# Kernel optimization log

Measured on AMD Instinct MI355X. Metric: run time of the kernel, lower is better.

## Reference

```python
import jax, jax.numpy as jnp
import numpy as np

V = 50000      # tokenizer vocab size
E = 128        # embedding_dim
H = 160        # encoder_hidden_dim (bidirectional -> 2H)
D = 196        # decoder_hidden_dim
A = 224        # attention_dim
BN = 56        # bottle_neck_dim
PAD, START, END, UNK = 0, 1, 2, 3
COV_FACTOR = 0.75


def _lstm_step(x, h, c, Wi, Wh, bi, bh):
    # torch gate order: i, f, g, o
    g = x @ Wi.T + h @ Wh.T + bi + bh
    i, f, gg, o = jnp.split(g, 4, axis=-1)
    c = jax.nn.sigmoid(f) * c + jax.nn.sigmoid(i) * jnp.tanh(gg)
    h = jax.nn.sigmoid(o) * jnp.tanh(c)
    return h, c


def _run_lstm(x_tbe, Wi, Wh, bi, bh):
    B = x_tbe.shape[1]
    Hh = Wh.shape[1]
    def step(carry, xt):
        h, c = carry
        h, c = _lstm_step(xt, h, c, Wi, Wh, bi, bh)
        return (h, c), h
    init = (jnp.zeros((B, Hh), x_tbe.dtype), jnp.zeros((B, Hh), x_tbe.dtype))
    (hT, cT), hs = jax.lax.scan(step, init, x_tbe)
    return hs, hT, cT


def setup_inputs() -> dict:
    key = jax.random.key(0)
    ks = iter(jax.random.split(key, 48))
    def rn(shape, s=0.05):
        return jax.random.normal(next(ks), shape, jnp.float32) * s
    B, Tin, Ttgt = 32, 256, 100
    inp = {
        'batch_input_ids': jax.random.randint(next(ks), (B, Tin), 0, V + 50, dtype=jnp.int32),
        'batch_target_ids': jax.random.randint(next(ks), (B, Ttgt), 0, V + 50, dtype=jnp.int32),
        'max_num_oovs': 50,
        'emb': rn((V, E), 0.1),
        # bidirectional encoder LSTM
        'Wi_f': rn((4 * H, E)), 'Wh_f': rn((4 * H, H)),
        'bi_f': jnp.zeros(4 * H), 'bh_f': jnp.zeros(4 * H),
        'Wi_b': rn((4 * H, E)), 'Wh_b': rn((4 * H, H)),
        'bi_b': jnp.zeros(4 * H), 'bh_b': jnp.zeros(4 * H),
        # enc->dec bridges
        'Weh': rn((D, 2 * H)), 'beh': jnp.zeros(D),
        'Wec': rn((D, 2 * H)), 'bec': jnp.zeros(D),
        # decoder LSTMCell
        'Wi_d': rn((4 * D, E)), 'Wh_d': rn((4 * D, D)),
        'bi_d': jnp.zeros(4 * D), 'bh_d': jnp.zeros(4 * D),
        # attention
        'Wea': rn((A, 2 * H)), 'bea': jnp.zeros(A),
        'Wda': rn((A, D)),
        'Wca': rn((A, 1)),
        'v_attn': rn((1, A)),
        # vocab projection (bottleneck)
        'W1': rn((BN, D + 2 * H)), 'b1': jnp.zeros(BN),
        'W2': rn((V - END, BN)), 'b2': jnp.zeros(V - END),
        # p_gen switch
        'Wcs': rn((1, 2 * H)), 'bcs': jnp.zeros(1),
        'Wds': rn((1, D)),
        'Wes': rn((1, E)),
    }
    return inp


def reference(batch_input_ids, batch_target_ids, max_num_oovs, emb,
              Wi_f, Wh_f, bi_f, bh_f, Wi_b, Wh_b, bi_b, bh_b,
              Weh, beh, Wec, bec, Wi_d, Wh_d, bi_d, bh_d,
              Wea, bea, Wda, Wca, v_attn, W1, b1, W2, b2,
              Wcs, bcs, Wds, Wes):
    B, Tin = batch_input_ids.shape
    # map OOV input ids to <unk> for embedding lookup
    in_mapped = jnp.where(batch_input_ids >= V, UNK, batch_input_ids)
    x_tbe = emb[in_mapped].transpose(1, 0, 2)          # [Tin,B,E]
    hs_f, hTf, cTf = _run_lstm(x_tbe, Wi_f, Wh_f, bi_f, bh_f)
    hs_b, hTb, cTb = _run_lstm(x_tbe[::-1], Wi_b, Wh_b, bi_b, bh_b)
    enc = jnp.concatenate([hs_f, hs_b[::-1]], -1).transpose(1, 0, 2)  # [B,Tin,2H]
    h = jnp.concatenate([hTf, hTb], -1) @ Weh.T + beh   # [B,D]
    c = jnp.concatenate([cTf, cTb], -1) @ Wec.T + bec   # [B,D]
    enc_attn = enc @ Wea.T + bea                        # [B,Tin,A] (loop-invariant)
    pad_mask = batch_input_ids == PAD
    wca = Wca[:, 0]                                     # [A]
    cov0 = jnp.zeros((B, Tin))
    cur0 = jnp.full((B,), START, jnp.int32)

    def step(carry, nt):
        h, c, cov, cur, nll, cl = carry
        e = emb[cur]                                     # [B,E]
        h, c = _lstm_step(e, h, c, Wi_d, Wh_d, bi_d, bh_d)
        s = jnp.tanh(enc_attn + (h @ Wda.T)[:, None, :] + cov[:, :, None] * wca)
        s = s @ v_attn[0]                                # [B,Tin]
        s = jnp.where(pad_mask, -jnp.inf, s)
        attn = jax.nn.softmax(s, axis=1)                 # [B,Tin]
        ctx = jnp.einsum('bt,bth->bh', attn, enc)        # [B,2H]
        hc = jnp.concatenate([h, ctx], -1)
        vocab = jax.nn.softmax(jnp.tanh(hc @ W1.T + b1) @ W2.T + b2, axis=1)  # [B,V-END]
        p_gen = jax.nn.sigmoid(ctx @ Wcs[0] + bcs[0] + h @ Wds[0] + e @ Wes[0])  # [B]
        # F.pad(vocab, (END, max_num_oovs)).gather(1, nt): left-pad END zeros,
        # right-pad OOV zeros -> gen prob is vocab[nt-END] if END<=nt<V else 0
        idx = jnp.clip(nt - END, 0, vocab.shape[1] - 1)
        gen_p = jnp.take_along_axis(vocab, idx[:, None], axis=1)[:, 0]
        gen_p = jnp.where((nt >= END) & (nt < V), gen_p, 0.0)
        copy_p = jnp.sum(attn * (batch_input_ids == nt[:, None]), axis=1)
        p = p_gen * gen_p + (1.0 - p_gen) * copy_p
        nll = nll - jnp.log(p + 1e-9)
        cl = cl + jnp.minimum(attn, cov).sum(axis=1)
        cov = cov + attn
        cur = jnp.where(nt >= V, UNK, nt)
        return (h, c, cov, cur, nll, cl), None

    (h, c, cov, cur, nll, cl), _ = jax.lax.scan(
        step, (h, c, cov0, cur0, jnp.zeros(B), jnp.zeros(B)), batch_target_ids.T)
    nll_loss = nll.sum()
    cov_loss = cl.sum()
    return nll_loss, cov_loss, nll_loss + COV_FACTOR * cov_loss
```

## Files before the change

kernel.cpp:

```cpp
#include <hip/hip_runtime.h>

#define MSCOPE __HIP_MEMORY_SCOPE_AGENT


constexpr size_t oXf   = 0;
constexpr size_t oXb   = oXf   + (size_t)8192*640;
constexpr size_t oXd   = oXb   + (size_t)8192*640;
constexpr size_t oHencB= oXd   + (size_t)3200*784;
constexpr size_t oEncA = oHencB+ (size_t)64*256*160;
constexpr size_t oEs   = oEncA + (size_t)8192*224;
constexpr size_t oCT   = oEs   + 3200;
constexpr size_t oH0   = oCT   + 10240;
constexpr size_t oC0   = oH0   + 6272;
constexpr size_t oHWdsAll = oC0 + 6272;
constexpr size_t oCtxWAll = oHWdsAll + 3200;
constexpr size_t oCopyAll = oCtxWAll + 3200;
constexpr size_t oZidxAll = oCopyAll + 3200;
constexpr size_t oClAll   = oZidxAll + 3200;
constexpr size_t oNllWg   = oClAll + 32;
constexpr size_t oW1cT    = oNllWg + 224;
constexpr size_t oFEnd    = oW1cT + 17920;
constexpr size_t oHdAll   = 0;
constexpr size_t oUAll    = oHdAll + (size_t)100*6272;
constexpr size_t oUPreAll = oUAll  + (size_t)100*1792;
constexpr size_t oHwdaAll = oUPreAll + (size_t)100*1792;
constexpr size_t oPartAll = oHwdaAll + (size_t)100*7168;
#define ENCW(d,t)  (((d)*256 + (t))*16)
#define FLSTM(s)   (8192 + (s)*16)
#define FAUX(s)    (9792 + (s)*16)
#define FP2W(s,m)  (11392 + (s)*64 + (m)*16)
#define CP3        17792
#define CFIN       17793
constexpr int fEnd = 17800;
constexpr unsigned ENC_FULL  = 0xFFFFFu;
constexpr unsigned LSTM_FULL = 0x1FFFFFFu;
constexpr unsigned AUX_FULL  = 0xFFu;
constexpr unsigned P2_FULL   = 0xFFFFFFFFu;

__device__ __forceinline__ float fast_tanh(float x){
  float e = __expf(-2.f*fabsf(x));
  float r = (1.f - e) * __builtin_amdgcn_rcpf(1.f + e);
  return copysignf(r, x);
}
__device__ __forceinline__ float sigm(float x){
  return __builtin_amdgcn_rcpf(1.f + __expf(-x));
}
__device__ __forceinline__ float aload(const float* p){
  return __hip_atomic_load(const_cast<float*>(p), __ATOMIC_RELAXED, MSCOPE);
}
__device__ __forceinline__ float2 aload2(const float* p){
  unsigned long long u = __hip_atomic_load(
      reinterpret_cast<unsigned long long*>(const_cast<float*>(p)),
      __ATOMIC_RELAXED, MSCOPE);
  float2 r; __builtin_memcpy(&r, &u, 8); return r;
}
__device__ __forceinline__ void astore(float* p, float v){
  __hip_atomic_store(p, v, __ATOMIC_RELAXED, MSCOPE);
}
template<int SLP>
__device__ __forceinline__ void wait_mask(unsigned* word, unsigned target, int tid){
  if (tid == 0){
    while (__hip_atomic_load(word, __ATOMIC_RELAXED, MSCOPE) != target)
      __builtin_amdgcn_s_sleep(SLP);
  }
  __syncthreads();
}
__device__ __forceinline__ void or_bit(unsigned* word, unsigned bit){
  (void)__hip_atomic_fetch_or(word, bit, __ATOMIC_RELAXED, MSCOPE);
}
__device__ __forceinline__ void add1(unsigned* word){
  (void)__hip_atomic_fetch_add(word, 1u, __ATOMIC_RELAXED, MSCOPE);
}
__device__ __forceinline__ float block_sum(float v, float* red){
  #pragma unroll
  for (int o=32;o;o>>=1) v += __shfl_down(v,o);
  if ((threadIdx.x&63)==0) red[threadIdx.x>>6] = v;
  __syncthreads();
  v = red[0]+red[1]+red[2]+red[3];
  __syncthreads();
  return v;
}

__global__ void prep_kernel(const int* __restrict__ in_ids, const int* __restrict__ tgt,
                            int* __restrict__ in_mapped, int* __restrict__ cur_ids,
                            unsigned* __restrict__ flags){
  int i = blockIdx.x*256 + threadIdx.x;
  if (i < 8192){
    int t = i >> 5, b = i & 31;
    int id = in_ids[b*256 + t];
    in_mapped[i] = (id >= 50000) ? 3 : id;
  }
  if (i < 3200){
    int k = i >> 5, b = i & 31;
    int id = (k == 0) ? 1 : tgt[b*100 + (k-1)];
    cur_ids[i] = (id >= 50000) ? 3 : id;
  }
  if (i < fEnd) flags[i] = 0u;
}

__global__ void w1c_transpose(const float* __restrict__ W1, float* __restrict__ W1cT){
  int i = blockIdx.x*256 + threadIdx.x;
  if (i < 17920){ int q = i / 56, g = i - q*56; W1cT[q*56+g] = W1[(size_t)g*516 + 196 + q]; }
}

struct RGArgs{ const int* gid; const float* emb; const float* W;
               const float* bias1; const float* bias2; float* out; int N; };
__global__ void __launch_bounds__(256) rowgemm(RGArgs a){
  __shared__ float rl[8*128];
  const int tid = threadIdx.x;
  const int N = a.N;
  const size_t r0 = (size_t)blockIdx.x*8;
  const size_t t = r0 >> 5; const int b0 = (int)(r0 & 31);
  for (int i = tid; i < 8*128; i += 256){
    int r = i >> 7, k = i & 127;
    rl[i] = a.emb[(size_t)a.gid[r0+r]*128 + k];
  }
  __syncthreads();
  for (int g = tid; g < N; g += 256){
    const float* wr = a.W + (size_t)g*128;
    float acc[8];
    #pragma unroll
    for (int r=0;r<8;r++) acc[r]=0.f;
    for (int k=0;k<128;k+=4){
      float4 wv = *(const float4*)(wr+k);
      #pragma unroll
      for (int r=0;r<8;r++){
        float4 xv = *(const float4*)(rl + r*128 + k);
        acc[r] += wv.x*xv.x + wv.y*xv.y + wv.z*xv.z + wv.w*xv.w;
      }
    }
    float bias = a.bias1[g] + a.bias2[g];
    float* op = a.out + ((size_t)t*N + g)*32 + b0;
    *(float4*)(op)   = make_float4(acc[0]+bias,acc[1]+bias,acc[2]+bias,acc[3]+bias);
    *(float4*)(op+4) = make_float4(acc[4]+bias,acc[5]+bias,acc[6]+bias,acc[7]+bias);
  }
}

__global__ void es_kernel(const int* __restrict__ gid, const float* __restrict__ emb,
                          const float* __restrict__ Wes, float* __restrict__ es){
  int r = blockIdx.x, l = threadIdx.x;
  const float* e = emb + (size_t)gid[r]*128;
  float acc = e[l]*Wes[l] + e[l+64]*Wes[l+64];
  #pragma unroll
  for (int o=32;o;o>>=1) acc += __shfl_down(acc,o);
  if (l==0) es[r] = acc;
}

struct EncArgs{ const float* Xf; const float* Xb; const float* Whf; const float* Whb;
                float* hencB; float* cT; unsigned* flg; };
__global__ void __launch_bounds__(256) enc_scan(EncArgs a){
  extern __shared__ float sm[];
  float* Wl = sm;
  float* hl = sm + 5120;
  const int wg = blockIdx.x;
  const int dir = wg/20, jwg = wg%20;
  const int tid = threadIdx.x;
  const int b = tid & 31, jl = tid >> 5;
  const int j = jwg*8 + jl;
  const float* Wh = dir ? a.Whb : a.Whf;
  const float* X  = dir ? a.Xb  : a.Xf;
  float* HB = a.hencB + (size_t)dir*32*256*160;
  unsigned* flg = a.flg;
  for (int i = tid; i < 32*160; i += 256){
    int row = i/160, k = i - row*160;
    int gate = row >> 3, jj = row & 7;
    Wl[i] = Wh[((size_t)(gate*160 + jwg*8 + jj))*160 + k];
  }
  for (int i = tid; i < 32*164; i += 256) hl[i] = 0.f;
  float c = 0.f;
  const float4* w0 = (const float4*)(Wl + (0*8+jl)*160);
  const float4* w1 = (const float4*)(Wl + (1*8+jl)*160);
  const float4* w2 = (const float4*)(Wl + (2*8+jl)*160);
  const float4* w3 = (const float4*)(Wl + (3*8+jl)*160);
  __syncthreads();
  for (int t = 0; t < 256; ++t){
    const int trow = dir ? 255 - t : t;
    const float* xr = X + ((size_t)trow*640 + j)*32 + b;
    float g0 = xr[0], g1 = xr[5120], g2 = xr[10240], g3 = xr[15360];
    if (t > 0){
      wait_mask<2>(flg + ENCW(dir, t-1), ENC_FULL, tid);
      const int tprev = dir ? (256 - t) : (t-1);
      for (int i2 = tid; i2 < 2560; i2 += 256){
        int bb = i2/80, kk = (i2 - bb*80)*2;
        float2 v = aload2(HB + ((size_t)bb*256 + tprev)*160 + kk);
        *(float2*)(hl + bb*164 + kk) = v;
      }
    }
    __syncthreads();
    const float4* hr = (const float4*)(hl + b*164);
    #pragma unroll 4
    for (int q = 0; q < 40; ++q){
      float4 hv = hr[q];
      float4 a0 = w0[q], a1 = w1[q], a2 = w2[q], a3 = w3[q];
      g0 += hv.x*a0.x + hv.y*a0.y + hv.z*a0.z + hv.w*a0.w;
      g1 += hv.x*a1.x + hv.y*a1.y + hv.z*a1.z + hv.w*a1.w;
      g2 += hv.x*a2.x + hv.y*a2.y + hv.z*a2.z + hv.w*a2.w;
      g3 += hv.x*a3.x + hv.y*a3.y + hv.z*a3.z + hv.w*a3.w;
    }
    float ig = sigm(g0), fg = sigm(g1), gc = fast_tanh(g2), og = sigm(g3);
    c = fg*c + ig*gc;
    float h = og * fast_tanh(c);
    astore(&HB[((size_t)b*256 + trow)*160 + j], h);
    __syncthreads();
    if (tid == 0) or_bit(flg + ENCW(dir, t), 1u << jwg);
  }
  a.cT[dir*5120 + b*160 + j] = c;
}

__global__ void mid_kernel(const float* __restrict__ hencB, const float* __restrict__ cT,
                           const float* __restrict__ Weh, const float* __restrict__ beh,
                           const float* __restrict__ Wec, const float* __restrict__ bec,
                           float* __restrict__ h0, float* __restrict__ c0){
  __shared__ float hc[320], cc[320];
  int b = blockIdx.x, tid = threadIdx.x;
  if (tid < 160){
    hc[tid]     = hencB[((size_t)b*256 + 255)*160 + tid];
    hc[160+tid] = hencB[((size_t)(32+b)*256 + 0)*160 + tid];
    cc[tid]     = cT[b*160 + tid];
    cc[160+tid] = cT[5120 + b*160 + tid];
  }
  __syncthreads();
  for (int g = tid; g < 196; g += 256){
    const float* w1 = Weh + (size_t)g*320;
    const float* w2 = Wec + (size_t)g*320;
    float a1 = beh[g], a2 = bec[g];
    for (int k = 0; k < 320; ++k){ a1 += hc[k]*w1[k]; a2 += cc[k]*w2[k]; }
    h0[b*196 + g] = a1;
    c0[b*196 + g] = a2;
  }
}

__global__ void __launch_bounds__(256) encA_gemm(const float* __restrict__ hencB,
                 const float* __restrict__ Wea, const float* __restrict__ bea,
                 float* __restrict__ encA){
  __shared__ float rl[8*320];
  const int tid = threadIdx.x;
  const size_t r0 = (size_t)blockIdx.x*8;
  for (int i = tid; i < 8*320; i += 256){
    int r = i/320, k = i - r*320;
    size_t row = r0 + r; int b = (int)(row >> 8), t = (int)(row & 255);
    rl[i] = (k < 160) ? hencB[((size_t)b*256 + t)*160 + k]
                      : hencB[((size_t)(32+b)*256 + t)*160 + (k-160)];
  }
  __syncthreads();
  for (int g = tid; g < 224; g += 256){
    const float* wr = Wea + (size_t)g*320;
    float acc[8];
    #pragma unroll
    for (int r=0;r<8;r++) acc[r]=0.f;
    for (int k=0;k<320;k+=4){
      float4 wv = *(const float4*)(wr+k);
      #pragma unroll
      for (int r=0;r<8;r++){
        float4 xv = *(const float4*)(rl + r*320 + k);
        acc[r] += wv.x*xv.x + wv.y*xv.y + wv.z*xv.z + wv.w*xv.w;
      }
    }
    float bias = bea[g];
    #pragma unroll
    for (int r=0;r<8;r++) encA[(r0+r)*224 + g] = acc[r] + bias;
  }
}

struct DecArgs{
  const float* Xd; const float* hencB; const float* encA;
  const float* h0; const float* c0;
  const float* Whd; const float* Wda; const float* Wca; const float* vat;
  const float* W1; const float* b1; const float* W1cT; const float* W2; const float* b2;
  const float* Wcs; const float* bcs; const float* Wds; const float* es;
  const int* in_ids; const int* tgt;
  float* hdAll; float* uAll; float* uPreAll; float* hwdaAll;
  float* hWdsAll; float* ctxWAll; float* copyAll;
  float* zidxAll; float* partAll; float* clAll; float* nllWg; float* out;
  unsigned* flg;
};

__device__ __forceinline__ void load_scr(const float* hp, float* scr, int tid){
  for (int i2 = tid; i2 < 3136; i2 += 256){
    float2 hv = aload2(hp + i2*2);
    int e = i2*2; int b2 = e & 31; int j2 = e >> 5;
    scr[b2*204 + j2]     = hv.x;
    scr[(b2+1)*204 + j2] = hv.y;
  }
}

__global__ void __launch_bounds__(256) dec_scan(DecArgs A){
  extern __shared__ float sm[];
  const int wg = blockIdx.x, tid = threadIdx.x;
  const int bp = tid & 31, jl = tid >> 5;
  unsigned* flg = A.flg;

  if (wg < 25){
    const int wl = wg;
    const int j = wl*8 + jl;
    float* Wl  = sm;
    float* scr = sm + 6272;
    for (int i = tid; i < 32*196; i += 256){
      int row = i/196, k = i - row*196;
      int gate = row >> 3, jj = row & 7;
      int jg = wl*8 + jj;
      Wl[i] = (jg < 196) ? A.Whd[((size_t)(gate*196 + jg))*196 + k] : 0.f;
    }
    float c = (j < 196) ? A.c0[bp*196 + j] : 0.f;
    for (int i = tid; i < 6272; i += 256){
      int bb = i/196, k = i - bb*196;
      scr[bb*204 + k] = A.h0[i];
    }
    const float4* w0 = (const float4*)(Wl + (0*8+jl)*196);
    const float4* w1 = (const float4*)(Wl + (1*8+jl)*196);
    const float4* w2 = (const float4*)(Wl + (2*8+jl)*196);
    const float4* w3 = (const float4*)(Wl + (3*8+jl)*196);
    __syncthreads();
    for (int s = 0; s < 100; ++s){
      float x0=0.f,x1=0.f,x2=0.f,x3=0.f;
      if (j < 196){
        const float* xr = A.Xd + ((size_t)s*784 + j)*32 + bp;
        x0 = xr[0]; x1 = xr[6272]; x2 = xr[12544]; x3 = xr[18816];
      }
      if (s > 0){
        wait_mask<2>(flg + FLSTM(s-1), LSTM_FULL, tid);
        load_scr(A.hdAll + (size_t)(s-1)*6272, scr, tid);
      }
      __syncthreads();
      if (j < 196){
        float g0=x0,g1=x1,g2=x2,g3=x3;
        const float4* hr = (const float4*)(scr + bp*204);
        #pragma unroll 7
        for (int q = 0; q < 49; ++q){
          float4 hv = hr[q];
          float4 a0 = w0[q], a1 = w1[q], a2 = w2[q], a3 = w3[q];
          g0 += hv.x*a0.x + hv.y*a0.y + hv.z*a0.z + hv.w*a0.w;
          g1 += hv.x*a1.x + hv.y*a1.y + hv.z*a1.z + hv.w*a1.w;
          g2 += hv.x*a2.x + hv.y*a2.y + hv.z*a2.z + hv.w*a2.w;
          g3 += hv.x*a3.x + hv.y*a3.y + hv.z*a3.z + hv.w*a3.w;
        }
        float ig = sigm(g0), fg = sigm(g1), gc = fast_tanh(g2), og = sigm(g3);
        c = fg*c + ig*gc;
        float h = og * fast_tanh(c);
        astore(&A.hdAll[(size_t)s*6272 + j*32 + bp], h);
      }
      __syncthreads();
      if (tid == 0) or_bit(flg + FLSTM(s), 1u << wl);
    }
    return;
  }

  if (wg < 33){
    const int a_ = wg - 25;
    float* wdaL = sm;
    float* w1hL = sm + 5488;
    float* WdsL = sm + 6860;
    float* scr  = sm + 7056;
    for (int i = tid; i < 28*196; i += 256){
      int al = i/196, k = i - al*196;
      wdaL[i] = A.Wda[(size_t)(a_*28 + al)*196 + k];
    }
    for (int i = tid; i < 7*196; i += 256){
      int gl = i/196, k = i - gl*196;
      w1hL[i] = A.W1[(size_t)(a_*7 + gl)*516 + k];
    }
    if (a_ == 7) for (int i = tid; i < 196; i += 256) WdsL[i] = A.Wds[i];
    __syncthreads();
    for (int s = 0; s < 100; ++s){
      wait_mask<2>(flg + FLSTM(s), LSTM_FULL, tid);
      load_scr(A.hdAll + (size_t)s*6272, scr, tid);
      __syncthreads();
      for (int i = tid; i < 896; i += 256){
        int b2 = i & 31, al = i >> 5;
        const float4* h4 = (const float4*)(scr + b2*204);
        const float4* w4 = (const float4*)(wdaL + al*196);
        float acc = 0.f;
        #pragma unroll 7
        for (int q = 0; q < 49; ++q){
          float4 a4 = h4[q], b4 = w4[q];
          acc += a4.x*b4.x + a4.y*b4.y + a4.z*b4.z + a4.w*b4.w;
        }
        astore(&A.hwdaAll[(size_t)s*7168 + b2*224 + a_*28 + al], acc);
      }
      if (tid < 224){
        int b2 = tid & 31, gl = tid >> 5;
        int g = a_*7 + gl;
        const float4* h4 = (const float4*)(scr + b2*204);
        const float4* w4 = (const float4*)(w1hL + gl*196);
        float acc = A.b1[g];
        #pragma unroll 7
        for (int q = 0; q < 49; ++q){
          float4 a4 = h4[q], b4 = w4[q];
          acc += a4.x*b4.x + a4.y*b4.y + a4.z*b4.z + a4.w*b4.w;
        }
        astore(&A.uPreAll[(size_t)s*1792 + b2*56 + g], acc);
      }
      if (a_ == 7 && tid < 32){
        const float* hb = scr + tid*204;
        float acc = 0.f;
        #pragma unroll 4
        for (int q = 0; q < 196; ++q) acc += hb[q]*WdsL[q];
        astore(&A.hWdsAll[s*32 + tid], acc);
      }
      __syncthreads();
      if (tid == 0) or_bit(flg + FAUX(s), 1u << a_);
    }
    return;
  }

  if (wg < 65){
    const int b = wg - 33;
    float* hwdaL = sm;
    float* attnL = sm + 224;
    float* pctx  = sm + 480;
    float* ctxL  = sm + 1440;
    float* red   = sm + 1760;
    float* pu    = sm + 1764;
    float* wcaL  = sm + 1988;
    float* vL    = sm + 2212;
    float* WcsL  = sm + 2436;
    if (tid < 224){ wcaL[tid] = A.Wca[tid]; vL[tid] = A.vat[tid]; }
    for (int i = tid; i < 320; i += 256) WcsL[i] = A.Wcs[i];
    const int inid = A.in_ids[b*256 + tid];
    const float4* erow = (const float4*)(A.encA + (size_t)(b*256 + tid)*224);
    float cov = 0.f, clr = 0.f;
    __syncthreads();
    for (int s = 0; s < 100; ++s){
      wait_mask<2>(flg + FAUX(s), AUX_FULL, tid);
      if (tid < 224) hwdaL[tid] = aload(&A.hwdaAll[(size_t)s*7168 + b*224 + tid]);
      __syncthreads();
      float exv = 0.f;
      if (inid != 0){
        float acc = 0.f;
        #pragma unroll 8
        for (int q = 0; q < 56; ++q){
          float4 ev = erow[q]; int a0 = 4*q;
          acc += fast_tanh(ev.x + hwdaL[a0]   + cov*wcaL[a0]  )*vL[a0];
          acc += fast_tanh(ev.y + hwdaL[a0+1] + cov*wcaL[a0+1])*vL[a0+1];
          acc += fast_tanh(ev.z + hwdaL[a0+2] + cov*wcaL[a0+2])*vL[a0+2];
          acc += fast_tanh(ev.w + hwdaL[a0+3] + cov*wcaL[a0+3])*vL[a0+3];
        }
        exv = __expf(acc);
      }
      float S = block_sum(exv, red);
      float attn = exv * __builtin_amdgcn_rcpf(S);
      attnL[tid] = attn;
      const int ntb = A.tgt[b*100 + s];
      float cpS = block_sum((inid == ntb) ? attn : 0.f, red);
      float mnS = block_sum(fminf(attn, cov), red);
      if (tid == 0){
        astore(&A.copyAll[s*32 + b], cpS);
        clr += mnS;
        if (s == 99) astore(&A.clAll[b], clr);
      }
      cov += attn;
      if (tid < 240){
        int seg = tid/80, h4i = tid - seg*80;
        int t0 = seg*86, t1 = (t0+86 < 256) ? t0+86 : 256;
        const float* base = (h4i < 40)
          ? (A.hencB + ((size_t)b*256)*160 + (size_t)h4i*4)
          : (A.hencB + ((size_t)(32+b)*256)*160 + (size_t)(h4i-40)*4);
        float4 accv = {0.f,0.f,0.f,0.f};
        #pragma unroll 4
        for (int t2 = t0; t2 < t1; ++t2){
          float av = attnL[t2];
          float4 ev = *(const float4*)(base + (size_t)t2*160);
          accv.x += av*ev.x; accv.y += av*ev.y; accv.z += av*ev.z; accv.w += av*ev.w;
        }
        *(float4*)(pctx + (seg*80+h4i)*4) = accv;
      }
      __syncthreads();
      if (tid < 80){
        float4 p0 = *(float4*)(pctx + tid*4);
        float4 p1 = *(float4*)(pctx + (80+tid)*4);
        float4 p2v = *(float4*)(pctx + (160+tid)*4);
        float4 cvv;
        cvv.x = p0.x+p1.x+p2v.x; cvv.y = p0.y+p1.y+p2v.y;
        cvv.z = p0.z+p1.z+p2v.z; cvv.w = p0.w+p1.w+p2v.w;
        *(float4*)(ctxL + tid*4) = cvv;
      }
      __syncthreads();
      if (tid < 224){
        int g = tid % 56, seg = tid / 56;
        float acc = 0.f;
        const float* wp = A.W1cT + (size_t)seg*80*56 + g;
        #pragma unroll 4
        for (int q = 0; q < 80; ++q) acc += ctxL[seg*80 + q] * wp[q*56];
        pu[seg*56 + g] = acc;
      } else {
        int l = tid - 224; float acc = 0.f;
        for (int q = l; q < 320; q += 32) acc += ctxL[q]*WcsL[q];
        #pragma unroll
        for (int o=16;o;o>>=1) acc += __shfl_down(acc,o,32);
        if (l==0) astore(&A.ctxWAll[s*32 + b], acc);
      }
      __syncthreads();
      if (tid < 56){
        float upre = aload(&A.uPreAll[(size_t)s*1792 + b*56 + tid]);
        float uu = fast_tanh(upre + pu[tid] + pu[56+tid] + pu[112+tid] + pu[168+tid]);
        astore(&A.uAll[(size_t)s*1792 + b*56 + tid], uu);
      }
      __syncthreads();
      if (tid == 0){
        or_bit(flg + FP2W(s,0), 1u << b);
        or_bit(flg + FP2W(s,1), 1u << b);
        or_bit(flg + FP2W(s,2), 1u << b);
        or_bit(flg + FP2W(s,3), 1u << b);
      }
    }
    return;
  }

  {
    const int wgv = wg - 65;
    const int vs = (wgv*49998)/224, ve = ((wgv+1)*49998)/224;
    const int v = vs + tid;
    const bool valid = v < ve;
    const int vc = valid ? v : 0;
    float4 w2r[14];
    {
      const float4* wr = (const float4*)(A.W2 + (size_t)vc*56);
      #pragma unroll
      for (int q=0;q<14;++q) w2r[q] = wr[q];
    }
    const float b2v = A.b2[vc];
    float* ulL  = sm;
    float* redW = sm + 1792;
    int*   idxL = (int*)(sm + 1920);
    float* red  = sm + 1952;
    const int lane = tid & 63, wv2 = tid >> 6;
    for (int s = 0; s < 100; ++s){
      int nt3 = (tid < 32) ? A.tgt[tid*100 + s] : 0;
      wait_mask<8>(flg + FP2W(s, wgv & 3), P2_FULL, tid);
      for (int i2 = tid; i2 < 896; i2 += 256){
        float2 u2 = aload2(&A.uAll[(size_t)s*1792 + i2*2]);
        *(float2*)(ulL + i2*2) = u2;
      }
      if (tid < 32){
        int ix = nt3 - 2; ix = ix<0?0:(ix>49997?49997:ix);
        idxL[tid] = ix;
      }
      __syncthreads();
      #pragma unroll 4
      for (int bb=0; bb<32; ++bb){
        const float4* uv = (const float4*)(ulL + bb*56);
        float z = b2v;
        #pragma unroll
        for (int q=0;q<14;++q){
          float4 u4 = uv[q];
          z += w2r[q].x*u4.x + w2r[q].y*u4.y + w2r[q].z*u4.z + w2r[q].w*u4.w;
        }
        if (valid && v == idxL[bb]) astore(&A.zidxAll[s*32+bb], z);
        float sv2 = valid ? __expf(z) : 0.f;
        #pragma unroll
        for (int o=32;o;o>>=1) sv2 += __shfl_down(sv2,o);
        if (lane == 0) redW[wv2*32+bb] = sv2;
      }
      __syncthreads();
      if (tid < 32){
        float tot = redW[tid]+redW[32+tid]+redW[64+tid]+redW[96+tid];
        astore(&A.partAll[(size_t)(s*32+tid)*224 + wgv], tot);
      }
      __syncthreads();
    }
    __syncthreads();
    if (tid == 0) add1(flg + CP3);
    if (tid == 0){
      while (__hip_atomic_load(flg + CP3, __ATOMIC_RELAXED, MSCOPE) != 224u)
        __builtin_amdgcn_s_sleep(32);
    }
    __syncthreads();
    float nll1 = 0.f;
    for (int p = wgv; p < 3200; p += 224){
      float pv = (tid < 224) ? aload(&A.partAll[(size_t)p*224 + tid]) : 0.f;
      float se = block_sum(pv, red);
      if (tid == 0){
        int s = p >> 5, b = p & 31;
        int nt2 = A.tgt[b*100 + s];
        float xg = aload(&A.ctxWAll[p]) + A.bcs[0] + aload(&A.hWdsAll[p]) + A.es[p];
        float pg = 1.f/(1.f + __expf(-xg));
        float genp = (nt2 >= 2 && nt2 < 50000) ? (__expf(aload(&A.zidxAll[p])) / se) : 0.f;
        float pr = pg*genp + (1.f-pg)*aload(&A.copyAll[p]);
        nll1 += -logf(pr + 1e-9f);
      }
    }
    if (tid == 0) astore(&A.nllWg[wgv], nll1);
    __syncthreads();
    if (tid == 0) add1(flg + CFIN);
    if (wg == 65){
      if (tid == 0){
        while (__hip_atomic_load(flg + CFIN, __ATOMIC_RELAXED, MSCOPE) != 224u)
          __builtin_amdgcn_s_sleep(32);
      }
      __syncthreads();
      float nv = (tid < 224) ? aload(&A.nllWg[tid]) : 0.f;
      float nll = block_sum(nv, red);
      float cv = (tid < 32) ? aload(&A.clAll[tid]) : 0.f;
      float cl = block_sum(cv, red);
      if (tid == 0){ A.out[0]=nll; A.out[1]=cl; A.out[2]=nll + 0.75f*cl; }
    }
  }
}

extern "C" void kernel_launch(void* const* d_in, const int* in_sizes, int n_in,
                              void* d_out, int out_size, void* d_ws, size_t ws_size,
                              hipStream_t stream){
  const int*   in_ids = (const int*)  d_in[0];
  const int*   tgt    = (const int*)  d_in[1];
  const float* emb    = (const float*)d_in[3];
  const float* Wi_f   = (const float*)d_in[4];
  const float* Wh_f   = (const float*)d_in[5];
  const float* bi_f   = (const float*)d_in[6];
  const float* bh_f   = (const float*)d_in[7];
  const float* Wi_b   = (const float*)d_in[8];
  const float* Wh_b   = (const float*)d_in[9];
  const float* bi_b   = (const float*)d_in[10];
  const float* bh_b   = (const float*)d_in[11];
  const float* Weh    = (const float*)d_in[12];
  const float* beh    = (const float*)d_in[13];
  const float* Wec    = (const float*)d_in[14];
  const float* bec    = (const float*)d_in[15];
  const float* Wi_d   = (const float*)d_in[16];
  const float* Wh_d   = (const float*)d_in[17];
  const float* bi_d   = (const float*)d_in[18];
  const float* bh_d   = (const float*)d_in[19];
  const float* Wea    = (const float*)d_in[20];
  const float* bea    = (const float*)d_in[21];
  const float* Wda    = (const float*)d_in[22];
  const float* Wca    = (const float*)d_in[23];
  const float* vat    = (const float*)d_in[24];
  const float* W1     = (const float*)d_in[25];
  const float* b1     = (const float*)d_in[26];
  const float* W2     = (const float*)d_in[27];
  const float* b2     = (const float*)d_in[28];
  const float* Wcs    = (const float*)d_in[29];
  const float* bcs    = (const float*)d_in[30];
  const float* Wds    = (const float*)d_in[31];
  const float* Wes    = (const float*)d_in[32];

  float* ws = (float*)d_ws;
  int* iBase = (int*)(ws + oFEnd);
  int* in_mapped = iBase;
  int* cur_ids   = iBase + 8192;
  unsigned* flags = (unsigned*)(iBase + 11392);

  prep_kernel<<<128, 256, 0, stream>>>(in_ids, tgt, in_mapped, cur_ids, flags);
  w1c_transpose<<<70, 256, 0, stream>>>(W1, ws + oW1cT);

  { RGArgs a{in_mapped, emb, Wi_f, bi_f, bh_f, ws + oXf, 640};
    rowgemm<<<1024, 256, 0, stream>>>(a); }
  { RGArgs a{in_mapped, emb, Wi_b, bi_b, bh_b, ws + oXb, 640};
    rowgemm<<<1024, 256, 0, stream>>>(a); }
  { RGArgs a{cur_ids, emb, Wi_d, bi_d, bh_d, ws + oXd, 784};
    rowgemm<<<400, 256, 0, stream>>>(a); }

  es_kernel<<<3200, 64, 0, stream>>>(cur_ids, emb, Wes, ws + oEs);

  { EncArgs ea{ws + oXf, ws + oXb, Wh_f, Wh_b, ws + oHencB, ws + oCT, flags};
    void* ka[] = {&ea};
    hipLaunchCooperativeKernel((void*)enc_scan, dim3(40), dim3(256), ka,
                               (unsigned)((5120 + 32*164)*4), stream); }

  mid_kernel<<<32, 256, 0, stream>>>(ws + oHencB, ws + oCT, Weh, beh, Wec, bec,
                                     ws + oH0, ws + oC0);

  encA_gemm<<<1024, 256, 0, stream>>>(ws + oHencB, Wea, bea, ws + oEncA);

  { DecArgs da{ws + oXd, ws + oHencB, ws + oEncA,
               ws + oH0, ws + oC0,
               Wh_d, Wda, Wca, vat,
               W1, b1, ws + oW1cT, W2, b2, Wcs, bcs, Wds, ws + oEs,
               in_ids, tgt,
               ws + oHdAll, ws + oUAll, ws + oUPreAll, ws + oHwdaAll,
               ws + oHWdsAll, ws + oCtxWAll, ws + oCopyAll,
               ws + oZidxAll, ws + oPartAll, ws + oClAll, ws + oNllWg, (float*)d_out,
               flags};
    void* ka[] = {&da};
    hipLaunchCooperativeKernel((void*)dec_scan, dim3(289), dim3(256), ka,
                               (unsigned)(13584*4), stream); }
}
```

Measured before the change: 4.651 ms.

## Replace atomic-OR bitmask flags with per-producer cache-line flags; shrink vocab WGs

Each producer workgroup now writes its own cache-line-padded flag instead of atomically OR-ing a bit into one shared word. Consumers poll all producer lines in parallel with one wavefront and a ballot, which removes contention on a single hot atomic. Separately, the vocab-projection stage drops from 224 to 191 workgroups, each handling two vocab rows per thread, so the cooperative decoder grid fits in 256 blocks. In exchange the flag array grows a lot, more memory must be zeroed in the prep kernel, and each vocab workgroup does more serial work per step.

```diff
diff --git a/kernel.cpp b/kernel.cpp
--- a/kernel.cpp
+++ b/kernel.cpp
@@ -18,24 +18,20 @@
 constexpr size_t oZidxAll = oCopyAll + 3200;
 constexpr size_t oClAll   = oZidxAll + 3200;
 constexpr size_t oNllWg   = oClAll + 32;
-constexpr size_t oW1cT    = oNllWg + 224;
+constexpr size_t oW1cT    = oNllWg + 192;
 constexpr size_t oFEnd    = oW1cT + 17920;
 constexpr size_t oHdAll   = 0;
 constexpr size_t oUAll    = oHdAll + (size_t)100*6272;
 constexpr size_t oUPreAll = oUAll  + (size_t)100*1792;
 constexpr size_t oHwdaAll = oUPreAll + (size_t)100*1792;
 constexpr size_t oPartAll = oHwdaAll + (size_t)100*7168;
-#define ENCW(d,t)  (((d)*256 + (t))*16)
-#define FLSTM(s)   (8192 + (s)*16)
-#define FAUX(s)    (9792 + (s)*16)
-#define FP2W(s,m)  (11392 + (s)*64 + (m)*16)
-#define CP3        17792
-#define CFIN       17793
-constexpr int fEnd = 17800;
-constexpr unsigned ENC_FULL  = 0xFFFFFu;
-constexpr unsigned LSTM_FULL = 0x1FFFFFFu;
-constexpr unsigned AUX_FULL  = 0xFFu;
-constexpr unsigned P2_FULL   = 0xFFFFFFFFu;
+#define FENC(d,t,p)  ((((d)*256 + (t))*20 + (p))*16)
+#define FLSTM(s,p)   (163840 + ((s)*25 + (p))*16)
+#define FAUX(s,p)    (203840 + ((s)*8 + (p))*16)
+#define FP2(s,m,p)   (216640 + (((s)*4 + (m))*32 + (p))*16)
+#define CP3          421440
+#define CFIN         421456
+constexpr int fEnd = 421472;
 
 __device__ __forceinline__ float fast_tanh(float x){
   float e = __expf(-2.f*fabsf(x));
@@ -57,16 +53,20 @@
 __device__ __forceinline__ void astore(float* p, float v){
   __hip_atomic_store(p, v, __ATOMIC_RELAXED, MSCOPE);
 }
+__device__ __forceinline__ void set_line(unsigned* line){
+  __hip_atomic_store(line, 1u, __ATOMIC_RELAXED, MSCOPE);
+}
 template<int SLP>
-__device__ __forceinline__ void wait_mask(unsigned* word, unsigned target, int tid){
-  if (tid == 0){
-    while (__hip_atomic_load(word, __ATOMIC_RELAXED, MSCOPE) != target)
+__device__ __forceinline__ void wait_lines(unsigned* base, int n, int tid){
+  if (tid < 64){
+    for(;;){
+      bool miss = (tid < n) &&
+        (__hip_atomic_load(base + tid*16, __ATOMIC_RELAXED, MSCOPE) == 0u);
+      if (__ballot(miss) == 0ULL) break;
       __builtin_amdgcn_s_sleep(SLP);
+    }
   }
   __syncthreads();
-}
-__device__ __forceinline__ void or_bit(unsigned* word, unsigned bit){
-  (void)__hip_atomic_fetch_or(word, bit, __ATOMIC_RELAXED, MSCOPE);
 }
 __device__ __forceinline__ void add1(unsigned* word){
   (void)__hip_atomic_fetch_add(word, 1u, __ATOMIC_RELAXED, MSCOPE);
@@ -84,18 +84,18 @@
 __global__ void prep_kernel(const int* __restrict__ in_ids, const int* __restrict__ tgt,
                             int* __restrict__ in_mapped, int* __restrict__ cur_ids,
                             unsigned* __restrict__ flags){
-  int i = blockIdx.x*256 + threadIdx.x;
-  if (i < 8192){
+  const int g0 = blockIdx.x*256 + threadIdx.x, stride = gridDim.x*256;
+  for (int i = g0; i < 8192; i += stride){
     int t = i >> 5, b = i & 31;
     int id = in_ids[b*256 + t];
     in_mapped[i] = (id >= 50000) ? 3 : id;
   }
-  if (i < 3200){
+  for (int i = g0; i < 3200; i += stride){
     int k = i >> 5, b = i & 31;
     int id = (k == 0) ? 1 : tgt[b*100 + (k-1)];
     cur_ids[i] = (id >= 50000) ? 3 : id;
   }
-  if (i < fEnd) flags[i] = 0u;
+  for (int i = g0; i < fEnd; i += stride) flags[i] = 0u;
 }
 
 __global__ void w1c_transpose(const float* __restrict__ W1, float* __restrict__ W1cT){
@@ -178,7 +178,7 @@
     const float* xr = X + ((size_t)trow*640 + j)*32 + b;
     float g0 = xr[0], g1 = xr[5120], g2 = xr[10240], g3 = xr[15360];
     if (t > 0){
-      wait_mask<2>(flg + ENCW(dir, t-1), ENC_FULL, tid);
+      wait_lines<2>(flg + FENC(dir, t-1, 0), 20, tid);
       const int tprev = dir ? (256 - t) : (t-1);
       for (int i2 = tid; i2 < 2560; i2 += 256){
         int bb = i2/80, kk = (i2 - bb*80)*2;
@@ -202,7 +202,7 @@
     float h = og * fast_tanh(c);
     astore(&HB[((size_t)b*256 + trow)*160 + j], h);
     __syncthreads();
-    if (tid == 0) or_bit(flg + ENCW(dir, t), 1u << jwg);
+    if (tid == 0) set_line(flg + FENC(dir, t, jwg));
   }
   a.cT[dir*5120 + b*160 + j] = c;
 }
@@ -318,7 +318,7 @@
         x0 = xr[0]; x1 = xr[6272]; x2 = xr[12544]; x3 = xr[18816];
       }
       if (s > 0){
-        wait_mask<2>(flg + FLSTM(s-1), LSTM_FULL, tid);
+        wait_lines<2>(flg + FLSTM(s-1, 0), 25, tid);
         load_scr(A.hdAll + (size_t)(s-1)*6272, scr, tid);
       }
       __syncthreads();
@@ -340,7 +340,7 @@
         astore(&A.hdAll[(size_t)s*6272 + j*32 + bp], h);
       }
       __syncthreads();
-      if (tid == 0) or_bit(flg + FLSTM(s), 1u << wl);
+      if (tid == 0) set_line(flg + FLSTM(s, wl));
     }
     return;
   }
@@ -362,7 +362,7 @@
     if (a_ == 7) for (int i = tid; i < 196; i += 256) WdsL[i] = A.Wds[i];
     __syncthreads();
     for (int s = 0; s < 100; ++s){
-      wait_mask<2>(flg + FLSTM(s), LSTM_FULL, tid);
+      wait_lines<2>(flg + FLSTM(s, 0), 25, tid);
       load_scr(A.hdAll + (size_t)s*6272, scr, tid);
       __syncthreads();
       for (int i = tid; i < 896; i += 256){
@@ -398,7 +398,7 @@
         astore(&A.hWdsAll[s*32 + tid], acc);
       }
       __syncthreads();
-      if (tid == 0) or_bit(flg + FAUX(s), 1u << a_);
+      if (tid == 0) set_line(flg + FAUX(s, a_));
     }
     return;
   }
@@ -421,7 +421,7 @@
     float cov = 0.f, clr = 0.f;
     __syncthreads();
     for (int s = 0; s < 100; ++s){
-      wait_mask<2>(flg + FAUX(s), AUX_FULL, tid);
+      wait_lines<2>(flg + FAUX(s, 0), 8, tid);
       if (tid < 224) hwdaL[tid] = aload(&A.hwdaAll[(size_t)s*7168 + b*224 + tid]);
       __syncthreads();
       float exv = 0.f;
@@ -497,10 +497,10 @@
       }
       __syncthreads();
       if (tid == 0){
-        or_bit(flg + FP2W(s,0), 1u << b);
-        or_bit(flg + FP2W(s,1), 1u << b);
-        or_bit(flg + FP2W(s,2), 1u << b);
-        or_bit(flg + FP2W(s,3), 1u << b);
+        set_line(flg + FP2(s,0,b));
+        set_line(flg + FP2(s,1,b));
+        set_line(flg + FP2(s,2,b));
+        set_line(flg + FP2(s,3,b));
       }
     }
     return;
@@ -508,17 +508,22 @@
 
   {
     const int wgv = wg - 65;
-    const int vs = (wgv*49998)/224, ve = ((wgv+1)*49998)/224;
-    const int v = vs + tid;
-    const bool valid = v < ve;
-    const int vc = valid ? v : 0;
-    float4 w2r[14];
+    const int vs = (int)(((long long)wgv*49998)/191);
+    const int ve = (int)(((long long)(wgv+1)*49998)/191);
+    const int r0v = vs + tid;
+    const int r1v = vs + 256 + tid;
+    const bool v1 = r1v < ve;
+    float4 w2r0[14], w2r1[14];
     {
-      const float4* wr = (const float4*)(A.W2 + (size_t)vc*56);
+      const float4* wr = (const float4*)(A.W2 + (size_t)r0v*56);
       #pragma unroll
-      for (int q=0;q<14;++q) w2r[q] = wr[q];
-    }
-    const float b2v = A.b2[vc];
+      for (int q=0;q<14;++q) w2r0[q] = wr[q];
+      const float4* wr1 = (const float4*)(A.W2 + (size_t)(v1 ? r1v : vs)*56);
+      #pragma unroll
+      for (int q=0;q<14;++q) w2r1[q] = wr1[q];
+    }
+    const float b2v0 = A.b2[r0v];
+    const float b2v1 = v1 ? A.b2[r1v] : 0.f;
     float* ulL  = sm;
     float* redW = sm + 1792;
     int*   idxL = (int*)(sm + 1920);
@@ -526,7 +531,7 @@
     const int lane = tid & 63, wv2 = tid >> 6;
     for (int s = 0; s < 100; ++s){
       int nt3 = (tid < 32) ? A.tgt[tid*100 + s] : 0;
-      wait_mask<8>(flg + FP2W(s, wgv & 3), P2_FULL, tid);
+      wait_lines<8>(flg + FP2(s, wgv & 3, 0), 32, tid);
       for (int i2 = tid; i2 < 896; i2 += 256){
         float2 u2 = aload2(&A.uAll[(size_t)s*1792 + i2*2]);
         *(float2*)(ulL + i2*2) = u2;
@@ -539,14 +544,24 @@
       #pragma unroll 4
       for (int bb=0; bb<32; ++bb){
         const float4* uv = (const float4*)(ulL + bb*56);
-        float z = b2v;
+        float z = b2v0;
         #pragma unroll
         for (int q=0;q<14;++q){
           float4 u4 = uv[q];
-          z += w2r[q].x*u4.x + w2r[q].y*u4.y + w2r[q].z*u4.z + w2r[q].w*u4.w;
+          z += w2r0[q].x*u4.x + w2r0[q].y*u4.y + w2r0[q].z*u4.z + w2r0[q].w*u4.w;
         }
-        if (valid && v == idxL[bb]) astore(&A.zidxAll[s*32+bb], z);
-        float sv2 = valid ? __expf(z) : 0.f;
+        if (r0v == idxL[bb]) astore(&A.zidxAll[s*32+bb], z);
+        float sv2 = __expf(z);
+        if (v1){
+          float z1 = b2v1;
+          #pragma unroll
+          for (int q=0;q<14;++q){
+            float4 u4 = uv[q];
+            z1 += w2r1[q].x*u4.x + w2r1[q].y*u4.y + w2r1[q].z*u4.z + w2r1[q].w*u4.w;
+          }
+          if (r1v == idxL[bb]) astore(&A.zidxAll[s*32+bb], z1);
+          sv2 += __expf(z1);
+        }
         #pragma unroll
         for (int o=32;o;o>>=1) sv2 += __shfl_down(sv2,o);
         if (lane == 0) redW[wv2*32+bb] = sv2;
@@ -554,20 +569,20 @@
       __syncthreads();
       if (tid < 32){
         float tot = redW[tid]+redW[32+tid]+redW[64+tid]+redW[96+tid];
-        astore(&A.partAll[(size_t)(s*32+tid)*224 + wgv], tot);
+        astore(&A.partAll[(size_t)(s*32+tid)*191 + wgv], tot);
       }
       __syncthreads();
     }
     __syncthreads();
     if (tid == 0) add1(flg + CP3);
     if (tid == 0){
-      while (__hip_atomic_load(flg + CP3, __ATOMIC_RELAXED, MSCOPE) != 224u)
+      while (__hip_atomic_load(flg + CP3, __ATOMIC_RELAXED, MSCOPE) != 191u)
         __builtin_amdgcn_s_sleep(32);
     }
     __syncthreads();
     float nll1 = 0.f;
-    for (int p = wgv; p < 3200; p += 224){
-      float pv = (tid < 224) ? aload(&A.partAll[(size_t)p*224 + tid]) : 0.f;
+    for (int p = wgv; p < 3200; p += 191){
+      float pv = (tid < 191) ? aload(&A.partAll[(size_t)p*191 + tid]) : 0.f;
       float se = block_sum(pv, red);
       if (tid == 0){
         int s = p >> 5, b = p & 31;
@@ -584,11 +599,11 @@
     if (tid == 0) add1(flg + CFIN);
     if (wg == 65){
       if (tid == 0){
-        while (__hip_atomic_load(flg + CFIN, __ATOMIC_RELAXED, MSCOPE) != 224u)
+        while (__hip_atomic_load(flg + CFIN, __ATOMIC_RELAXED, MSCOPE) != 191u)
           __builtin_amdgcn_s_sleep(32);
       }
       __syncthreads();
-      float nv = (tid < 224) ? aload(&A.nllWg[tid]) : 0.f;
+      float nv = (tid < 191) ? aload(&A.nllWg[tid]) : 0.f;
       float nll = block_sum(nv, red);
       float cv = (tid < 32) ? aload(&A.clAll[tid]) : 0.f;
       float cl = block_sum(cv, red);
@@ -639,7 +654,7 @@
   int* cur_ids   = iBase + 8192;
   unsigned* flags = (unsigned*)(iBase + 11392);
 
-  prep_kernel<<<128, 256, 0, stream>>>(in_ids, tgt, in_mapped, cur_ids, flags);
+  prep_kernel<<<512, 256, 0, stream>>>(in_ids, tgt, in_mapped, cur_ids, flags);
   w1c_transpose<<<70, 256, 0, stream>>>(W1, ws + oW1cT);
 
   { RGArgs a{in_mapped, emb, Wi_f, bi_f, bh_f, ws + oXf, 640};
@@ -671,6 +686,6 @@
                ws + oZidxAll, ws + oPartAll, ws + oClAll, ws + oNllWg, (float*)d_out,
                flags};
     void* ka[] = {&da};
-    hipLaunchCooperativeKernel((void*)dec_scan, dim3(289), dim3(256), ka,
+    hipLaunchCooperativeKernel((void*)dec_scan, dim3(256), dim3(256), ka,
                                (unsigned)(13584*4), stream); }
 }
```

After: 4.925 ms. 1.06x slower.
